# Kernel tuning notes

Measured on AMD Instinct MI355X. Metric: run time of the kernel, lower is better.

Reference implementation:

```python
import jax, jax.numpy as jnp
import numpy as np

B, D, STRIDE, OUT = 8192, 1024, 16, 64
L = D // STRIDE


def setup_inputs() -> dict:
    key = jax.random.key(0)
    kx, kw, kb = jax.random.split(key, 3)
    x = jax.random.normal(kx, (B, D), dtype=jnp.float32)
    # Stacked per-layer Dense kernels: layer i only sees features j < i*STRIDE.
    # Glorot-ish scale; masked entries are zeroed in reference() (faithful: they
    # don't exist in the original per-layer kernels).
    W = jax.random.normal(kw, (L, D, OUT), dtype=jnp.float32) * 0.02
    b = jax.random.normal(kb, (L, OUT), dtype=jnp.float32) * 0.02
    return {"x": x, "W": W, "b": b}


def reference(x, W, b):
    # Original: tf.stack([Dense_i(x[..., :i*stride]) for i in range(L)], -2)
    # Equivalent single causal-masked batched matmul.
    Lx, Dx, Ox = W.shape
    stride = Dx // Lx
    # mask[l, d] = 1 if feature d is visible to layer l (d < l*stride)
    mask = (jnp.arange(Dx)[None, :] < (jnp.arange(Lx) * stride)[:, None]).astype(W.dtype)
    Wm = W * mask[:, :, None]                      # [L, D, O]
    out = jnp.einsum("bd,ldo->blo", x, Wm) + b    # [B, L, O]
    return out
```

## Files before the change

kernel.cpp:

```cpp
#include <hip/hip_runtime.h>
#include <hip/hip_bf16.h>
#include <stdint.h>

#define BROWS 8192
#define DDIM  1024
#define LDIM  64
#define ODIM  64
#define NDIM  4096
#define KSTRIDE 16

typedef __attribute__((ext_vector_type(8))) short bf16x8;
typedef __attribute__((ext_vector_type(4))) float f32x4;
typedef __attribute__((ext_vector_type(8))) unsigned short u16x8;

static __device__ __forceinline__ unsigned short f2bf(float f) {
    union { float f; uint32_t u; } v; v.f = f;
    uint32_t r = 0x7FFFu + ((v.u >> 16) & 1u);
    return (unsigned short)((v.u + r) >> 16);
}

static __device__ __forceinline__ void async16(const void* g, void* l) {
    __builtin_amdgcn_global_load_lds(
        (const __attribute__((address_space(1))) void*)g,
        (__attribute__((address_space(3))) void*)l, 16, 0, 0);
}

__global__ __launch_bounds__(256) void prep_kernel(const float* __restrict__ x,
                                                   const float* __restrict__ W,
                                                   unsigned short* __restrict__ xb,
                                                   unsigned short* __restrict__ wbt) {
    const int bid = blockIdx.x;
    if (bid < 1024) {
        __shared__ float tile[64][65];
        const int l  = bid >> 4;
        const int d0 = (bid & 15) << 6;
        const int t  = threadIdx.x;
        {
            const int dd = t >> 2;
            const int o4 = (t & 3) << 4;
            const float* src = W + ((size_t)((l << 10) + d0 + dd) << 6) + o4;
            #pragma unroll
            for (int j = 0; j < 4; ++j) {
                float4 v = reinterpret_cast<const float4*>(src)[j];
                tile[dd][o4 + 4 * j + 0] = v.x;
                tile[dd][o4 + 4 * j + 1] = v.y;
                tile[dd][o4 + 4 * j + 2] = v.z;
                tile[dd][o4 + 4 * j + 3] = v.w;
            }
        }
        __syncthreads();
        {
            const int o    = t >> 2;
            const int dloc = (t & 3) << 4;
            const int kmax = l * KSTRIDE;
            unsigned short* dst = wbt + ((size_t)((l << 6) + o) << 10) + d0 + dloc;
            u16x8 r0, r1;
            #pragma unroll
            for (int j = 0; j < 8; ++j) {
                int da = d0 + dloc + j;
                int db = da + 8;
                r0[j] = (da < kmax) ? f2bf(tile[dloc + j][o])     : (unsigned short)0;
                r1[j] = (db < kmax) ? f2bf(tile[dloc + 8 + j][o]) : (unsigned short)0;
            }
            *reinterpret_cast<u16x8*>(dst)     = r0;
            *reinterpret_cast<u16x8*>(dst + 8) = r1;
        }
    } else {
        int i = (bid - 1024) * 256 + threadIdx.x;
        const float4* xf = reinterpret_cast<const float4*>(x);
        float4 v0 = xf[2 * i];
        float4 v1 = xf[2 * i + 1];
        u16x8 r;
        r[0] = f2bf(v0.x); r[1] = f2bf(v0.y); r[2] = f2bf(v0.z); r[3] = f2bf(v0.w);
        r[4] = f2bf(v1.x); r[5] = f2bf(v1.y); r[6] = f2bf(v1.z); r[7] = f2bf(v1.w);
        reinterpret_cast<u16x8*>(xb)[i] = r;
    }
}

__global__ __launch_bounds__(512, 2) void ar_gemm_kernel(
        const unsigned short* __restrict__ xb,
        const unsigned short* __restrict__ wbt,
        const float* __restrict__ bias,
        float* __restrict__ out) {
    __shared__ char lds[73728];

    const int s  = blockIdx.x >> 8;
    const int i  = blockIdx.x & 255;
    const int bm = ((s & 1) << 4) + (i & 15);
    const int bn = ((s < 2) ? 16 : 0) + 15 - (i >> 4);
    const int tid  = threadIdx.x;
    const int lane = tid & 63;
    const int wid  = tid >> 6;
    const int wm   = wid >> 1;
    const int wn   = wid & 1;

    const int nkt = bn + 1;

    const int cb = (tid & 3) << 4;
    const char* gA = (const char*)xb  + ((size_t)((bm << 8) + (tid >> 2)) << 11) + cb;
    const char* gB = (const char*)wbt + ((size_t)((bn << 7) + (tid >> 2)) << 11) + cb;

    const int aoff = ((wm << 6) + (lane & 15)) * 64 + ((lane >> 4) << 4);
    const int boff = 16384 + ((wn << 6) + (lane & 15)) * 64 + ((lane >> 4) << 4);

    f32x4 acc[4][4];
    #pragma unroll
    for (int m = 0; m < 4; ++m)
        #pragma unroll
        for (int n = 0; n < 4; ++n)
            acc[m][n] = (f32x4)(0.f);

    auto stage = [&](int t) {
        const int kb = (t < nkt ? t : nkt - 1) << 6;
        char* l = lds + (t % 3) * 24576 + tid * 16;
        async16(gA + kb, l);
        async16(gA + ((size_t)128 << 11) + kb, l + 8192);
        async16(gB + kb, l + 16384);
    };

    stage(0);
    stage(1);

    for (int t = 0; t < nkt; ++t) {
        asm volatile("s_waitcnt vmcnt(3)" ::: "memory");
        __builtin_amdgcn_sched_barrier(0);
        __builtin_amdgcn_s_barrier();
        stage(t + 2);
        const char* pb = lds + (t % 3) * 24576;
        bf16x8 a[4], b[4];
        #pragma unroll
        for (int m = 0; m < 4; ++m)
            a[m] = *reinterpret_cast<const bf16x8*>(pb + aoff + m * 1024);
        #pragma unroll
        for (int n = 0; n < 4; ++n)
            b[n] = *reinterpret_cast<const bf16x8*>(pb + boff + n * 1024);
        #pragma unroll
        for (int m = 0; m < 4; ++m)
            #pragma unroll
            for (int n = 0; n < 4; ++n)
                acc[m][n] = __builtin_amdgcn_mfma_f32_16x16x32_bf16(a[m], b[n], acc[m][n], 0, 0, 0);
    }
    asm volatile("s_waitcnt vmcnt(0)" ::: "memory");

    const int crow = (bm << 8) + (wm << 6) + ((lane >> 4) << 2);
    const int ccol = (bn << 7) + (wn << 6) + (lane & 15);
    float bv[4];
    #pragma unroll
    for (int n = 0; n < 4; ++n) bv[n] = bias[ccol + n * 16];
    #pragma unroll
    for (int m = 0; m < 4; ++m)
        #pragma unroll
        for (int n = 0; n < 4; ++n)
            #pragma unroll
            for (int j = 0; j < 4; ++j)
                out[(size_t)(crow + m * 16 + j) * NDIM + ccol + n * 16] = acc[m][n][j] + bv[n];
}

__global__ __launch_bounds__(256) void naive_kernel(const float* __restrict__ x,
                                                    const float* __restrict__ W,
                                                    const float* __restrict__ bias,
                                                    float* __restrict__ out) {
    size_t idx = (size_t)blockIdx.x * 256 + threadIdx.x;
    if (idx >= (size_t)BROWS * NDIM) return;
    int m = (int)(idx >> 12);
    int n = (int)(idx & 4095);
    int l = n >> 6;
    int o = n & 63;
    int kmax = l * KSTRIDE;
    float s = bias[n];
    const float* xr = x + (size_t)m * DDIM;
    const float* wp = W + ((size_t)l << 16) + o;
    for (int d = 0; d < kmax; ++d) s += xr[d] * wp[(size_t)d << 6];
    out[idx] = s;
}

extern "C" void kernel_launch(void* const* d_in, const int* in_sizes, int n_in,
                              void* d_out, int out_size, void* d_ws, size_t ws_size,
                              hipStream_t stream) {
    const float* x = (const float*)d_in[0];
    const float* W = (const float*)d_in[1];
    const float* b = (const float*)d_in[2];
    float* out = (float*)d_out;

    const size_t need = ((size_t)BROWS * DDIM + (size_t)NDIM * DDIM) * sizeof(unsigned short);
    if (ws_size < need) {
        int total = BROWS * NDIM;
        naive_kernel<<<(total + 255) / 256, 256, 0, stream>>>(x, W, b, out);
        return;
    }
    unsigned short* xbuf = (unsigned short*)d_ws;
    unsigned short* wbt  = xbuf + (size_t)BROWS * DDIM;

    prep_kernel<<<5120, 256, 0, stream>>>(x, W, xbuf, wbt);
    ar_gemm_kernel<<<1024, 512, 0, stream>>>(xbuf, wbt, b, out);
}
```

Measured before the change: 62.67 us.

## Double-buffer LDS fragment reads in registers and deepen async prefetch

Restructures the GEMM main loop so LDS fragments for the next k-step are read into a second register set while MFMAs run on the current set. The global-to-LDS prefetch distance grows from two stages to three, still within the three LDS buffers. MFMA issue is wrapped in s_setprio to favour the math waves. This aims to hide LDS read latency behind matrix work, at the cost of more VGPRs for the extra fragment set, which could hurt occupancy.

```diff
diff --git a/kernel.cpp b/kernel.cpp
--- a/kernel.cpp
+++ b/kernel.cpp
@@ -77,11 +77,39 @@
     }
 }
 
-__global__ __launch_bounds__(512, 2) void ar_gemm_kernel(
-        const unsigned short* __restrict__ xb,
-        const unsigned short* __restrict__ wbt,
-        const float* __restrict__ bias,
-        float* __restrict__ out) {
+#define MMQ(A, B) \
+    _Pragma("unroll") \
+    for (int m = 0; m < 4; ++m) \
+    _Pragma("unroll") \
+    for (int n = 0; n < 4; ++n) \
+        acc[m][n] = __builtin_amdgcn_mfma_f32_16x16x32_bf16(A[m], B[n], acc[m][n], 0, 0, 0);
+
+#define READF(T, A, B) do { \
+    const char* pb_ = lds + ((T) % 3) * 24576; \
+    _Pragma("unroll") \
+    for (int m = 0; m < 4; ++m) A[m] = *reinterpret_cast<const bf16x8*>(pb_ + aoff + m * 1024); \
+    _Pragma("unroll") \
+    for (int n = 0; n < 4; ++n) B[n] = *reinterpret_cast<const bf16x8*>(pb_ + boff + n * 1024); \
+} while (0)
+
+#define PHASE(T, Acur, Bcur, Anxt, Bnxt) \
+    asm volatile("s_waitcnt vmcnt(3)" ::: "memory");    \
+    __builtin_amdgcn_sched_barrier(0); \
+    __builtin_amdgcn_s_barrier();                       \
+    stage((T) + 3);                                     \
+    READF((T) + 1, Anxt, Bnxt);                         \
+    __builtin_amdgcn_sched_barrier(0); \
+    __builtin_amdgcn_s_setprio(1); \
+    MMQ(Acur, Bcur); \
+    __builtin_amdgcn_s_setprio(0); \
+    asm volatile("s_waitcnt lgkmcnt(0)" ::: "memory");
+
+__global__ __launch_bounds__(512)
+__attribute__((amdgpu_waves_per_eu(2)))
+void ar_gemm_kernel(const unsigned short* __restrict__ xb,
+                    const unsigned short* __restrict__ wbt,
+                    const float* __restrict__ bias,
+                    float* __restrict__ out) {
     __shared__ char lds[73728];
 
     const int s  = blockIdx.x >> 8;
@@ -110,6 +138,8 @@
         for (int n = 0; n < 4; ++n)
             acc[m][n] = (f32x4)(0.f);
 
+    bf16x8 aA[4], bA[4], aB[4], bB[4];
+
     auto stage = [&](int t) {
         const int kb = (t < nkt ? t : nkt - 1) << 6;
         char* l = lds + (t % 3) * 24576 + tid * 16;
@@ -118,27 +148,18 @@
         async16(gB + kb, l + 16384);
     };
 
-    stage(0);
-    stage(1);
-
-    for (int t = 0; t < nkt; ++t) {
-        asm volatile("s_waitcnt vmcnt(3)" ::: "memory");
-        __builtin_amdgcn_sched_barrier(0);
-        __builtin_amdgcn_s_barrier();
-        stage(t + 2);
-        const char* pb = lds + (t % 3) * 24576;
-        bf16x8 a[4], b[4];
-        #pragma unroll
-        for (int m = 0; m < 4; ++m)
-            a[m] = *reinterpret_cast<const bf16x8*>(pb + aoff + m * 1024);
-        #pragma unroll
-        for (int n = 0; n < 4; ++n)
-            b[n] = *reinterpret_cast<const bf16x8*>(pb + boff + n * 1024);
-        #pragma unroll
-        for (int m = 0; m < 4; ++m)
-            #pragma unroll
-            for (int n = 0; n < 4; ++n)
-                acc[m][n] = __builtin_amdgcn_mfma_f32_16x16x32_bf16(a[m], b[n], acc[m][n], 0, 0, 0);
+    stage(0); stage(1); stage(2);
+    asm volatile("s_waitcnt vmcnt(6)" ::: "memory");
+    __builtin_amdgcn_s_barrier();
+    READF(0, aA, bA);
+    asm volatile("s_waitcnt lgkmcnt(0)" ::: "memory");
+
+    int t = 0;
+    while (true) {
+        PHASE(t, aA, bA, aB, bB);
+        if (++t >= nkt) break;
+        PHASE(t, aB, bB, aA, bA);
+        if (++t >= nkt) break;
     }
     asm volatile("s_waitcnt vmcnt(0)" ::: "memory");
 
```

After: 69.59 us. 1.11x slower.

## Fuse x fp32-to-bf16 conversion into GEMM A-tile loading

Applied to the files above, without the earlier changes.

Removes the separate x-to-bf16 prep pass and workspace buffer. The GEMM now loads fp32 x rows into registers, converts them with v_cvt_pk_bf16_f32 and writes the A tile to LDS one stage ahead, while the B tile still uses async global-to-LDS loads. It also adds s_setprio around the MFMA block and drops the occupancy hint of 2 from launch_bounds. This avoids a global round trip for x but doubles the bytes of A read per K-tile, adds register pressure and conversion work inside the main loop, and the A tile is re-read across N tiles in fp32.

```diff
diff --git a/kernel.cpp b/kernel.cpp
--- a/kernel.cpp
+++ b/kernel.cpp
@@ -25,64 +25,52 @@
         (__attribute__((address_space(3))) void*)l, 16, 0, 0);
 }
 
-__global__ __launch_bounds__(256) void prep_kernel(const float* __restrict__ x,
-                                                   const float* __restrict__ W,
-                                                   unsigned short* __restrict__ xb,
+__global__ __launch_bounds__(256) void prep_kernel(const float* __restrict__ W,
                                                    unsigned short* __restrict__ wbt) {
+    __shared__ float tile[64][65];
     const int bid = blockIdx.x;
-    if (bid < 1024) {
-        __shared__ float tile[64][65];
-        const int l  = bid >> 4;
-        const int d0 = (bid & 15) << 6;
-        const int t  = threadIdx.x;
-        {
-            const int dd = t >> 2;
-            const int o4 = (t & 3) << 4;
-            const float* src = W + ((size_t)((l << 10) + d0 + dd) << 6) + o4;
-            #pragma unroll
-            for (int j = 0; j < 4; ++j) {
-                float4 v = reinterpret_cast<const float4*>(src)[j];
-                tile[dd][o4 + 4 * j + 0] = v.x;
-                tile[dd][o4 + 4 * j + 1] = v.y;
-                tile[dd][o4 + 4 * j + 2] = v.z;
-                tile[dd][o4 + 4 * j + 3] = v.w;
-            }
+    const int l  = bid >> 4;
+    const int d0 = (bid & 15) << 6;
+    const int t  = threadIdx.x;
+    {
+        const int dd = t >> 2;
+        const int o4 = (t & 3) << 4;
+        const float* src = W + ((size_t)((l << 10) + d0 + dd) << 6) + o4;
+        #pragma unroll
+        for (int j = 0; j < 4; ++j) {
+            float4 v = reinterpret_cast<const float4*>(src)[j];
+            tile[dd][o4 + 4 * j + 0] = v.x;
+            tile[dd][o4 + 4 * j + 1] = v.y;
+            tile[dd][o4 + 4 * j + 2] = v.z;
+            tile[dd][o4 + 4 * j + 3] = v.w;
         }
-        __syncthreads();
-        {
-            const int o    = t >> 2;
-            const int dloc = (t & 3) << 4;
-            const int kmax = l * KSTRIDE;
-            unsigned short* dst = wbt + ((size_t)((l << 6) + o) << 10) + d0 + dloc;
-            u16x8 r0, r1;
-            #pragma unroll
-            for (int j = 0; j < 8; ++j) {
-                int da = d0 + dloc + j;
-                int db = da + 8;
-                r0[j] = (da < kmax) ? f2bf(tile[dloc + j][o])     : (unsigned short)0;
-                r1[j] = (db < kmax) ? f2bf(tile[dloc + 8 + j][o]) : (unsigned short)0;
-            }
-            *reinterpret_cast<u16x8*>(dst)     = r0;
-            *reinterpret_cast<u16x8*>(dst + 8) = r1;
+    }
+    __syncthreads();
+    {
+        const int o    = t >> 2;
+        const int dloc = (t & 3) << 4;
+        const int kmax = l * KSTRIDE;
+        unsigned short* dst = wbt + ((size_t)((l << 6) + o) << 10) + d0 + dloc;
+        u16x8 r0, r1;
+        #pragma unroll
+        for (int j = 0; j < 8; ++j) {
+            int da = d0 + dloc + j;
+            int db = da + 8;
+            r0[j] = (da < kmax) ? f2bf(tile[dloc + j][o])     : (unsigned short)0;
+            r1[j] = (db < kmax) ? f2bf(tile[dloc + 8 + j][o]) : (unsigned short)0;
         }
-    } else {
-        int i = (bid - 1024) * 256 + threadIdx.x;
-        const float4* xf = reinterpret_cast<const float4*>(x);
-        float4 v0 = xf[2 * i];
-        float4 v1 = xf[2 * i + 1];
-        u16x8 r;
-        r[0] = f2bf(v0.x); r[1] = f2bf(v0.y); r[2] = f2bf(v0.z); r[3] = f2bf(v0.w);
-        r[4] = f2bf(v1.x); r[5] = f2bf(v1.y); r[6] = f2bf(v1.z); r[7] = f2bf(v1.w);
-        reinterpret_cast<u16x8*>(xb)[i] = r;
-    }
-}
-
-__global__ __launch_bounds__(512, 2) void ar_gemm_kernel(
-        const unsigned short* __restrict__ xb,
+        *reinterpret_cast<u16x8*>(dst)     = r0;
+        *reinterpret_cast<u16x8*>(dst + 8) = r1;
+    }
+}
+
+__global__ __launch_bounds__(512) void ar_gemm_kernel(
+        const float* __restrict__ x,
         const unsigned short* __restrict__ wbt,
         const float* __restrict__ bias,
         float* __restrict__ out) {
-    __shared__ char lds[73728];
+    __shared__ int4 smem[4608];
+    char* lds = (char*)smem;
 
     const int s  = blockIdx.x >> 8;
     const int i  = blockIdx.x & 255;
@@ -96,9 +84,10 @@
 
     const int nkt = bn + 1;
 
-    const int cb = (tid & 3) << 4;
-    const char* gA = (const char*)xb  + ((size_t)((bm << 8) + (tid >> 2)) << 11) + cb;
-    const char* gB = (const char*)wbt + ((size_t)((bn << 7) + (tid >> 2)) << 11) + cb;
+    const int rowA = tid >> 1, hA = tid & 1;
+    const float* gA = x + ((size_t)((bm << 8) + rowA) << 10) + (hA << 4);
+    const int ldsAoff = rowA * 64 + hA * 32;
+    const char* gB = (const char*)wbt + ((size_t)((bn << 7) + (tid >> 2)) << 11) + ((tid & 3) << 4);
 
     const int aoff = ((wm << 6) + (lane & 15)) * 64 + ((lane >> 4) << 4);
     const int boff = 16384 + ((wn << 6) + (lane & 15)) * 64 + ((lane >> 4) << 4);
@@ -110,35 +99,66 @@
         for (int n = 0; n < 4; ++n)
             acc[m][n] = (f32x4)(0.f);
 
-    auto stage = [&](int t) {
+    auto loadA = [&](int t, float4* r) {
+        const float* g = gA + ((size_t)(t < nkt ? t : nkt - 1) << 5);
+        #pragma unroll
+        for (int j = 0; j < 4; ++j)
+            r[j] = *reinterpret_cast<const float4*>(g + 4 * j);
+    };
+    auto cvtwriteA = [&](int t, const float4* r) {
+        char* dst = lds + (t % 3) * 24576 + ldsAoff;
+        const float* f = reinterpret_cast<const float*>(r);
+        int p[8];
+        #pragma unroll
+        for (int j = 0; j < 8; ++j)
+            asm("v_cvt_pk_bf16_f32 %0, %1, %2" : "=v"(p[j]) : "v"(f[2 * j]), "v"(f[2 * j + 1]));
+        *reinterpret_cast<int4*>(dst)      = make_int4(p[0], p[1], p[2], p[3]);
+        *reinterpret_cast<int4*>(dst + 16) = make_int4(p[4], p[5], p[6], p[7]);
+    };
+    auto stageB = [&](int t) {
         const int kb = (t < nkt ? t : nkt - 1) << 6;
-        char* l = lds + (t % 3) * 24576 + tid * 16;
-        async16(gA + kb, l);
-        async16(gA + ((size_t)128 << 11) + kb, l + 8192);
-        async16(gB + kb, l + 16384);
+        async16(gB + kb, lds + (t % 3) * 24576 + 16384 + tid * 16);
     };
 
-    stage(0);
-    stage(1);
+    float4 a0[4], ar[4];
+    loadA(0, a0); stageB(0);
+    loadA(1, ar); stageB(1);
+    cvtwriteA(0, a0);
+    asm volatile("s_waitcnt vmcnt(5)" ::: "memory");
+    asm volatile("s_waitcnt lgkmcnt(0)" ::: "memory");
+    __builtin_amdgcn_sched_barrier(0);
+    __builtin_amdgcn_s_barrier();
+    __builtin_amdgcn_sched_barrier(0);
 
     for (int t = 0; t < nkt; ++t) {
-        asm volatile("s_waitcnt vmcnt(3)" ::: "memory");
-        __builtin_amdgcn_sched_barrier(0);
-        __builtin_amdgcn_s_barrier();
-        stage(t + 2);
+        stageB(t + 2);
+        float4 an[4];
+        loadA(t + 2, an);
         const char* pb = lds + (t % 3) * 24576;
-        bf16x8 a[4], b[4];
+        bf16x8 afr[4], bfr[4];
         #pragma unroll
         for (int m = 0; m < 4; ++m)
-            a[m] = *reinterpret_cast<const bf16x8*>(pb + aoff + m * 1024);
+            afr[m] = *reinterpret_cast<const bf16x8*>(pb + aoff + m * 1024);
         #pragma unroll
         for (int n = 0; n < 4; ++n)
-            b[n] = *reinterpret_cast<const bf16x8*>(pb + boff + n * 1024);
+            bfr[n] = *reinterpret_cast<const bf16x8*>(pb + boff + n * 1024);
+        __builtin_amdgcn_s_setprio(1);
         #pragma unroll
         for (int m = 0; m < 4; ++m)
             #pragma unroll
             for (int n = 0; n < 4; ++n)
-                acc[m][n] = __builtin_amdgcn_mfma_f32_16x16x32_bf16(a[m], b[n], acc[m][n], 0, 0, 0);
+                acc[m][n] = __builtin_amdgcn_mfma_f32_16x16x32_bf16(afr[m], bfr[n], acc[m][n], 0, 0, 0);
+        __builtin_amdgcn_s_setprio(0);
+        cvtwriteA(t + 1, ar);
+        #pragma unroll
+        for (int j = 0; j < 4; ++j) ar[j] = an[j];
+        asm volatile("s_waitcnt lgkmcnt(0)" ::: "memory");
+        if (t + 1 < nkt) {
+            asm volatile("s_waitcnt vmcnt(5)" ::: "memory");
+            __builtin_amdgcn_sched_barrier(0);
+            __builtin_amdgcn_s_barrier();
+            __builtin_amdgcn_sched_barrier(0);
+        }
     }
     asm volatile("s_waitcnt vmcnt(0)" ::: "memory");
 
@@ -182,15 +202,14 @@
     const float* b = (const float*)d_in[2];
     float* out = (float*)d_out;
 
-    const size_t need = ((size_t)BROWS * DDIM + (size_t)NDIM * DDIM) * sizeof(unsigned short);
+    const size_t need = (size_t)NDIM * DDIM * sizeof(unsigned short);
     if (ws_size < need) {
         int total = BROWS * NDIM;
         naive_kernel<<<(total + 255) / 256, 256, 0, stream>>>(x, W, b, out);
         return;
     }
-    unsigned short* xbuf = (unsigned short*)d_ws;
-    unsigned short* wbt  = xbuf + (size_t)BROWS * DDIM;
-
-    prep_kernel<<<5120, 256, 0, stream>>>(x, W, xbuf, wbt);
-    ar_gemm_kernel<<<1024, 512, 0, stream>>>(xbuf, wbt, b, out);
-}
+    unsigned short* wbt = (unsigned short*)d_ws;
+
+    prep_kernel<<<1024, 256, 0, stream>>>(W, wbt);
+    ar_gemm_kernel<<<1024, 512, 0, stream>>>(x, wbt, b, out);
+}
```

Result: slower. 91.31 us (+45.7%).

## Split GEMM main loop into two ping-pong phases with interleaved async loads

Applied to the files above, without the earlier changes.

Restructures the K-loop so the A tiles and half the B fragments are read from LDS, then the next stage's A loads are issued, followed by half the MFMAs. After that the remaining B fragments are read, the B load is issued and the rest of the MFMAs run. Barriers and s_setprio bracket the MFMA clusters so waves alternate between memory and math phases. This aims to overlap global→LDS traffic and LDS reads with matrix core work, at the cost of extra barriers per iteration and more fragile synchronisation of the triple-buffered LDS.

```diff
diff --git a/kernel.cpp b/kernel.cpp
--- a/kernel.cpp
+++ b/kernel.cpp
@@ -110,35 +110,61 @@
         for (int n = 0; n < 4; ++n)
             acc[m][n] = (f32x4)(0.f);
 
-    auto stage = [&](int t) {
+    auto stageA2 = [&](int t) {
         const int kb = (t < nkt ? t : nkt - 1) << 6;
         char* l = lds + (t % 3) * 24576 + tid * 16;
         async16(gA + kb, l);
         async16(gA + ((size_t)128 << 11) + kb, l + 8192);
-        async16(gB + kb, l + 16384);
     };
-
-    stage(0);
-    stage(1);
+    auto stageB1 = [&](int t) {
+        const int kb = (t < nkt ? t : nkt - 1) << 6;
+        async16(gB + kb, lds + (t % 3) * 24576 + 16384 + tid * 16);
+    };
+
+    stageA2(0); stageB1(0);
+    stageA2(1); stageB1(1);
+    asm volatile("s_waitcnt vmcnt(3)" ::: "memory");
+    __builtin_amdgcn_sched_barrier(0);
+    __builtin_amdgcn_s_barrier();
 
     for (int t = 0; t < nkt; ++t) {
-        asm volatile("s_waitcnt vmcnt(3)" ::: "memory");
-        __builtin_amdgcn_sched_barrier(0);
-        __builtin_amdgcn_s_barrier();
-        stage(t + 2);
         const char* pb = lds + (t % 3) * 24576;
-        bf16x8 a[4], b[4];
+        bf16x8 a[4], b0, b1;
         #pragma unroll
         for (int m = 0; m < 4; ++m)
             a[m] = *reinterpret_cast<const bf16x8*>(pb + aoff + m * 1024);
-        #pragma unroll
-        for (int n = 0; n < 4; ++n)
-            b[n] = *reinterpret_cast<const bf16x8*>(pb + boff + n * 1024);
-        #pragma unroll
-        for (int m = 0; m < 4; ++m)
-            #pragma unroll
-            for (int n = 0; n < 4; ++n)
-                acc[m][n] = __builtin_amdgcn_mfma_f32_16x16x32_bf16(a[m], b[n], acc[m][n], 0, 0, 0);
+        b0 = *reinterpret_cast<const bf16x8*>(pb + boff);
+        b1 = *reinterpret_cast<const bf16x8*>(pb + boff + 1024);
+        stageA2(t + 2);
+        __builtin_amdgcn_s_barrier();
+        asm volatile("s_waitcnt lgkmcnt(0)" ::: "memory");
+        __builtin_amdgcn_sched_barrier(0);
+        __builtin_amdgcn_s_setprio(1);
+        #pragma unroll
+        for (int m = 0; m < 4; ++m) {
+            acc[m][0] = __builtin_amdgcn_mfma_f32_16x16x32_bf16(a[m], b0, acc[m][0], 0, 0, 0);
+            acc[m][1] = __builtin_amdgcn_mfma_f32_16x16x32_bf16(a[m], b1, acc[m][1], 0, 0, 0);
+        }
+        __builtin_amdgcn_s_setprio(0);
+        __builtin_amdgcn_sched_barrier(0);
+        __builtin_amdgcn_s_barrier();
+        bf16x8 b2, b3;
+        b2 = *reinterpret_cast<const bf16x8*>(pb + boff + 2048);
+        b3 = *reinterpret_cast<const bf16x8*>(pb + boff + 3072);
+        stageB1(t + 2);
+        __builtin_amdgcn_s_barrier();
+        asm volatile("s_waitcnt lgkmcnt(0)" ::: "memory");
+        __builtin_amdgcn_sched_barrier(0);
+        __builtin_amdgcn_s_setprio(1);
+        #pragma unroll
+        for (int m = 0; m < 4; ++m) {
+            acc[m][2] = __builtin_amdgcn_mfma_f32_16x16x32_bf16(a[m], b2, acc[m][2], 0, 0, 0);
+            acc[m][3] = __builtin_amdgcn_mfma_f32_16x16x32_bf16(a[m], b3, acc[m][3], 0, 0, 0);
+        }
+        __builtin_amdgcn_s_setprio(0);
+        asm volatile("s_waitcnt vmcnt(3)" ::: "memory");
+        __builtin_amdgcn_sched_barrier(0);
+        __builtin_amdgcn_s_barrier();
     }
     asm volatile("s_waitcnt vmcnt(0)" ::: "memory");
 
```

Result: no change. 62.91 us (+0.4%).
